# Kernel optimization log

Measured on AMD Instinct MI355X. Metric: run time of the kernel, lower is better.

## Reference

```python
import jax, jax.numpy as jnp
import numpy as np

T, B, D, H = 1024, 256, 256, 256


def setup_inputs() -> dict:
    key = jax.random.key(0)
    k1, k2, k3, k4 = jax.random.split(key, 4)
    ins = jax.random.normal(k1, (T, B, D), dtype=jnp.float32)
    resets = jax.random.randint(k2, (T, B), 0, 2).astype(jnp.bool_)
    init_h = jnp.zeros((B, H), dtype=jnp.float32)
    # packed GRU weights in (r, z, n) order; flax GRUCell: input dense has no
    # bias, hidden dense has bias, and r gates (Wh_n @ h + b_n).
    Wi = jax.random.normal(k3, (D, 3 * H), dtype=jnp.float32) / np.sqrt(D)
    Wh = jax.random.normal(k4, (H, 3 * H), dtype=jnp.float32) / np.sqrt(H)
    b = jnp.zeros((3 * H,), dtype=jnp.float32)
    return {"ins": ins, "resets": resets, "init_h": init_h,
            "Wi": Wi, "Wh": Wh, "b": b}


def reference(ins, resets, init_h, Wi, Wh, b):
    def step(h, xt):
        x, reset = xt                                  # x: [B,D], reset: [B]
        h = jnp.where(reset[:, None], jnp.zeros_like(h), h)
        gi = x @ Wi                                    # [B,3H] (no input bias)
        gh = h @ Wh + b                                # [B,3H] (hidden bias)
        ir, iz, i_n = jnp.split(gi, 3, axis=-1)
        hr, hz, h_n = jnp.split(gh, 3, axis=-1)
        r = jax.nn.sigmoid(ir + hr)
        z = jax.nn.sigmoid(iz + hz)
        n = jnp.tanh(i_n + r * h_n)                    # r gates (Wh_n h + b_n)
        new_h = (1.0 - z) * n + z * h
        return new_h, new_h                            # GRU: y == new hidden

    h_final, ys = jax.lax.scan(step, init_h, (ins, resets))
    return ys                                          # [T,B,H]
```

## Files before the change

kernel.cpp:

```cpp
#include <hip/hip_runtime.h>


typedef __attribute__((ext_vector_type(8))) short sv8;
typedef __attribute__((ext_vector_type(4))) short sv4;
typedef __attribute__((ext_vector_type(4))) float fv4;

#define HPAD 264
#define GAP 40

static __device__ __forceinline__ unsigned short f2bf(float f) {
  unsigned int u = __float_as_uint(f);
  u += 0x7fffu + ((u >> 16) & 1u);
  return (unsigned short)(u >> 16);
}
static __device__ __forceinline__ float bf2f(unsigned short s) {
  return __uint_as_float(((unsigned int)s) << 16);
}

__global__ __launch_bounds__(256) void transpose_w(
    const float* __restrict__ Wi, const float* __restrict__ Wh,
    unsigned short* __restrict__ Wt, unsigned short* __restrict__ Wht) {
  __shared__ float tile[32][33];
  const int bid = blockIdx.x;
  const float* src = (bid < 192) ? Wi : Wh;
  unsigned short* dst = (bid < 192) ? Wt : Wht;
  const int local = bid % 192;
  const int c0 = (local % 24) * 32;
  const int k0 = (local / 24) * 32;
  const int t = threadIdx.x, tr = t >> 5, tc = t & 31;
#pragma unroll
  for (int p = 0; p < 4; ++p) {
    int k = tr + p * 8;
    tile[k][tc] = src[(size_t)(k0 + k) * 768 + c0 + tc];
  }
  __syncthreads();
#pragma unroll
  for (int p = 0; p < 4; ++p) {
    int c = tr + p * 8;
    dst[(size_t)(c0 + c) * 256 + k0 + tc] = f2bf(tile[tc][c]);
  }
}

__global__ __launch_bounds__(256) void gi_gemm(
    const float* __restrict__ ins, const unsigned short* __restrict__ Wt,
    unsigned short* __restrict__ gi, int w0) {
  __shared__ __align__(16) unsigned short As[128][GAP];
  __shared__ __align__(16) unsigned short Bs[128][GAP];
  const int t = threadIdx.x;
  const int m0 = blockIdx.x * 128;
  const int n0 = blockIdx.y * 128;
  const int wave = t >> 6, lane = t & 63;
  const int n16 = lane & 15, quad = lane >> 4;
  const int m0w = (wave & 1) * 64, n0w = (wave >> 1) * 64;

  fv4 acc[4][4] = {};
  for (int kb = 0; kb < 8; ++kb) {
#pragma unroll
    for (int r = 0; r < 4; ++r) {
      const int m = (t >> 3) + r * 32;
      const int kk = (t & 7) * 4;
      const int grow = m0 + m;
      const float* xp = ins + ((size_t)(w0 + (grow >> 8)) * 256 + (grow & 255)) * 256 + kb * 32 + kk;
      fv4 v = *(const fv4*)xp;
      sv4 pk = {(short)f2bf(v[0]), (short)f2bf(v[1]), (short)f2bf(v[2]), (short)f2bf(v[3])};
      *(sv4*)&As[m][kk] = pk;
    }
    {
      const int n = t >> 1, kh = (t & 1) * 16;
      const sv8* wp = (const sv8*)(Wt + (size_t)(n0 + n) * 256 + kb * 32 + kh);
      *(sv8*)&Bs[n][kh] = wp[0];
      *(sv8*)&Bs[n][kh + 8] = wp[1];
    }
    __syncthreads();
    sv8 af[4], bfr[4];
#pragma unroll
    for (int mt = 0; mt < 4; ++mt) af[mt] = *(const sv8*)&As[m0w + mt * 16 + n16][quad * 8];
#pragma unroll
    for (int nt = 0; nt < 4; ++nt) bfr[nt] = *(const sv8*)&Bs[n0w + nt * 16 + n16][quad * 8];
#pragma unroll
    for (int mt = 0; mt < 4; ++mt)
#pragma unroll
      for (int nt = 0; nt < 4; ++nt)
        acc[mt][nt] = __builtin_amdgcn_mfma_f32_16x16x32_bf16(af[mt], bfr[nt], acc[mt][nt], 0, 0, 0);
    __syncthreads();
  }
#pragma unroll
  for (int mt = 0; mt < 4; ++mt)
#pragma unroll
    for (int i = 0; i < 4; ++i) {
      const int row = m0 + m0w + mt * 16 + quad * 4 + i;
      unsigned short* gp = gi + (size_t)row * 768 + n0 + n0w + n16;
#pragma unroll
      for (int nt = 0; nt < 4; ++nt) gp[nt * 16] = f2bf(acc[mt][nt][i]);
    }
}

__global__ __launch_bounds__(512, 2) void rec_kernel(
    const unsigned short* __restrict__ gi,
    const int* __restrict__ resets,
    const float* __restrict__ h_in,
    float* __restrict__ h_carry,
    const unsigned short* __restrict__ Wht,
    const float* __restrict__ bias,
    float* __restrict__ out,
    int t0, int wsteps) {
  __shared__ __align__(16) unsigned short whn[256][HPAD];
  __shared__ __align__(16) unsigned short hbuf[2][16][HPAD];
  __shared__ int rstl[1024];
  __shared__ int cand[16];
  __shared__ int cstart[17];
  __shared__ int s_smax;

  const int tid = threadIdx.x;
  const int wave = tid >> 6, lane = tid & 63;
  const int n16 = lane & 15, quad = lane >> 4;
  const int b = blockIdx.x;
  const int wcb = wave * 16;

  for (int e = tid; e < 8192; e += 512) {
    const int col = e >> 5, kc = (e & 31) * 8;
    *(sv8*)&whn[col][kc] = *(const sv8*)(Wht + (size_t)(512 + col) * 256 + kc);
  }
  for (int e = tid; e < wsteps; e += 512)
    rstl[e] = resets[(size_t)(t0 + e) * 256 + b];
  if (tid < 16) cand[tid] = wsteps;
  __syncthreads();

  {
    int span = wsteps >> 4;
    if (span < 1) span = 1;
    for (int e = tid; e < wsteps; e += 512)
      if (rstl[e]) {
        const int j = e / span;
        if (j < 16) atomicMin(&cand[j], e);
      }
  }
  {
    const int row = tid >> 5, c8 = (tid & 31) * 8;
    sv8 pk = {0, 0, 0, 0, 0, 0, 0, 0};
    if (row == 0 && !rstl[0]) {
      fv4 v0 = *(const fv4*)(h_in + (size_t)b * 256 + c8);
      fv4 v1 = *(const fv4*)(h_in + (size_t)b * 256 + c8 + 4);
#pragma unroll
      for (int j = 0; j < 4; ++j) pk[j] = (short)f2bf(v0[j]);
#pragma unroll
      for (int j = 0; j < 4; ++j) pk[4 + j] = (short)f2bf(v1[j]);
    }
    *(sv8*)&hbuf[0][row][c8] = pk;
  }
  __syncthreads();
  if (tid == 0) {
    int span = wsteps >> 4;
    if (span < 1) span = 1;
    int S[17];
    S[16] = wsteps;
    for (int j = 15; j >= 0; --j) S[j] = (cand[j] < wsteps) ? cand[j] : S[j + 1];
    int cnt = 1;
    cstart[0] = 0;
    for (int r = 1; r < 16; ++r) {
      const int v = S[r];
      if (v < wsteps && v > cstart[cnt - 1]) cstart[cnt++] = v;
    }
    for (int r = cnt; r <= 16; ++r) cstart[r] = wsteps;
    int mx = 0;
    for (int r = 0; r < 16; ++r) {
      const int L = cstart[r + 1] - cstart[r];
      if (L > mx) mx = L;
    }
    s_smax = mx;
  }
  __syncthreads();

  int rs_[4], rl_[4];
#pragma unroll
  for (int i = 0; i < 4; ++i) {
    const int ri = quad * 4 + i;
    rs_[i] = cstart[ri];
    rl_[i] = cstart[ri + 1] - rs_[i];
  }
  float hprev[4][2];
#pragma unroll
  for (int i = 0; i < 4; ++i)
#pragma unroll
    for (int c = 0; c < 2; ++c)
      hprev[i][c] = (rs_[i] == 0) ? h_in[(size_t)b * 256 + c * 128 + wcb + n16] : 0.f;

  sv8 whf[2][2][8];
#pragma unroll
  for (int g = 0; g < 2; ++g)
#pragma unroll
    for (int c = 0; c < 2; ++c)
#pragma unroll
      for (int kt = 0; kt < 8; ++kt)
        whf[g][c][kt] = *(const sv8*)(Wht + (size_t)(g * 256 + c * 128 + wcb + n16) * 256 + kt * 32 + quad * 8);

  float b_r[2], b_z[2], b_n[2];
#pragma unroll
  for (int c = 0; c < 2; ++c) {
    const int col = c * 128 + wcb + n16;
    b_r[c] = bias[col];
    b_z[c] = bias[256 + col];
    b_n[c] = bias[512 + col];
  }

  const unsigned short* gbase = gi + (size_t)b * 768 + wcb + n16;
  float* ob0 = out + (size_t)t0 * 65536 + (size_t)b * 256 + wcb + n16;
  const int smax = s_smax;

  auto prefetch = [&](int s, unsigned short (&dst)[2][3][4]) {
#pragma unroll
    for (int i = 0; i < 4; ++i) {
      int lt = rs_[i] + s;
      if (lt > wsteps - 1) lt = wsteps - 1;
      const unsigned short* g0 = gbase + (size_t)lt * 196608;
#pragma unroll
      for (int c = 0; c < 2; ++c) {
        dst[c][0][i] = g0[c * 128];
        dst[c][1][i] = g0[c * 128 + 256];
        dst[c][2][i] = g0[c * 128 + 512];
      }
    }
  };

  auto step = [&](int s, unsigned short (&cur)[2][3][4], unsigned short (&nxt)[2][3][4]) {
    const int rb = s & 1, wb = rb ^ 1;
    fv4 acc[3][2] = {};
#pragma unroll
    for (int kt = 0; kt < 8; ++kt) {
      sv8 hf = *(const sv8*)&hbuf[rb][n16][kt * 32 + quad * 8];
#pragma unroll
      for (int c = 0; c < 2; ++c) {
        sv8 wnf = *(const sv8*)&whn[c * 128 + wcb + n16][kt * 32 + quad * 8];
        acc[0][c] = __builtin_amdgcn_mfma_f32_16x16x32_bf16(hf, whf[0][c][kt], acc[0][c], 0, 0, 0);
        acc[1][c] = __builtin_amdgcn_mfma_f32_16x16x32_bf16(hf, whf[1][c][kt], acc[1][c], 0, 0, 0);
        acc[2][c] = __builtin_amdgcn_mfma_f32_16x16x32_bf16(hf, wnf, acc[2][c], 0, 0, 0);
      }
    }
    prefetch(s + 1, nxt);
#pragma unroll
    for (int i = 0; i < 4; ++i) {
      const int lt = rs_[i] + s;
      const bool act = (s < rl_[i]);
      const int rcur = act ? rstl[lt] : 1;
      const int nf = (s + 1 < rl_[i]) ? rstl[lt + 1] : 1;
#pragma unroll
      for (int c = 0; c < 2; ++c) {
        const float pre_r = bf2f(cur[c][0][i]) + acc[0][c][i] + b_r[c];
        const float pre_z = bf2f(cur[c][1][i]) + acc[1][c][i] + b_z[c];
        const float r = __builtin_amdgcn_rcpf(1.f + __expf(-pre_r));
        const float z = __builtin_amdgcn_rcpf(1.f + __expf(-pre_z));
        const float npre = bf2f(cur[c][2][i]) + r * (acc[2][c][i] + b_n[c]);
        const float n = 1.f - 2.f * __builtin_amdgcn_rcpf(1.f + __expf(2.f * npre));
        const float hp = rcur ? 0.f : hprev[i][c];
        const float hnew = (1.f - z) * n + z * hp;
        hprev[i][c] = hnew;
        if (act) {
          ob0[(size_t)lt * 65536 + c * 128] = hnew;
          if (lt == wsteps - 1) h_carry[(size_t)b * 256 + c * 128 + wcb + n16] = hnew;
        }
        hbuf[wb][quad * 4 + i][c * 128 + wcb + n16] = nf ? (unsigned short)0 : f2bf(hnew);
      }
    }
    __builtin_amdgcn_sched_barrier(0);
    asm volatile("s_waitcnt lgkmcnt(0)" ::: "memory");
    __builtin_amdgcn_s_barrier();
    __builtin_amdgcn_sched_barrier(0);
  };

  unsigned short A_[2][3][4], B_[2][3][4];
  prefetch(0, A_);
  for (int s = 0; s < smax; s += 2) {
    step(s, A_, B_);
    if (s + 1 < smax) step(s + 1, B_, A_);
  }
}

extern "C" void kernel_launch(void* const* d_in, const int* in_sizes, int n_in,
                              void* d_out, int out_size, void* d_ws, size_t ws_size,
                              hipStream_t stream) {
  const float* ins    = (const float*)d_in[0];
  const int* resets   = (const int*)d_in[1];
  const float* init_h = (const float*)d_in[2];
  const float* Wi     = (const float*)d_in[3];
  const float* Wh     = (const float*)d_in[4];
  const float* bias   = (const float*)d_in[5];
  float* out          = (float*)d_out;

  char* ws = (char*)d_ws;
  unsigned short* Wt  = (unsigned short*)ws;
  unsigned short* Wht = (unsigned short*)(ws + 393216);
  float* h_carry      = (float*)(ws + 786432);
  unsigned short* gi  = (unsigned short*)(ws + 1048576);

  int wsteps = 1024;
  while (wsteps > 2 && (size_t)1048576 + (size_t)wsteps * 256 * 768 * 2 > ws_size) wsteps >>= 1;
  const int nwin = 1024 / wsteps;

  hipLaunchKernelGGL(transpose_w, dim3(384), dim3(256), 0, stream, Wi, Wh, Wt, Wht);
  for (int w = 0; w < nwin; ++w) {
    const int t0 = w * wsteps;
    hipLaunchKernelGGL(gi_gemm, dim3(wsteps * 2, 6), dim3(256), 0, stream, ins, Wt, gi, t0);
    hipLaunchKernelGGL(rec_kernel, dim3(256), dim3(512), 0, stream,
                       gi, resets, (w == 0 ? init_h : h_carry), h_carry, Wht, bias, out, t0, wsteps);
  }
}
```

Baseline: 1.062 ms.

## Pre-convert inputs to bf16, use direct global-to-LDS loads, defer recurrence stores

Adds a separate pass that converts the fp32 inputs to bf16 once. The input-projection GEMM now stages tiles with global_load_lds directly into a blocked LDS layout and swaps the grid axes so neighbouring blocks share A rows. In the recurrent kernel, gate prefetch uses incrementing pointers, the reset flag is carried between steps, and output and h_carry stores are moved after the barrier so they stay off the critical path. The trade is an extra 128MB of workspace and a full read/write pass over the inputs, and the workspace check may shrink the window size.

```diff
diff --git a/kernel.cpp b/kernel.cpp
--- a/kernel.cpp
+++ b/kernel.cpp
@@ -6,7 +6,6 @@
 typedef __attribute__((ext_vector_type(4))) float fv4;
 
 #define HPAD 264
-#define GAP 40
 
 static __device__ __forceinline__ unsigned short f2bf(float f) {
   unsigned int u = __float_as_uint(f);
@@ -15,6 +14,12 @@
 }
 static __device__ __forceinline__ float bf2f(unsigned short s) {
   return __uint_as_float(((unsigned int)s) << 16);
+}
+
+static __device__ __forceinline__ void gload16(const void* g, void* l) {
+  __builtin_amdgcn_global_load_lds((__attribute__((address_space(1))) void*)g,
+                                   (__attribute__((address_space(3))) void*)l,
+                                   16, 0, 0);
 }
 
 __global__ __launch_bounds__(256) void transpose_w(
@@ -41,42 +46,61 @@
   }
 }
 
-__global__ __launch_bounds__(256) void gi_gemm(
-    const float* __restrict__ ins, const unsigned short* __restrict__ Wt,
+__global__ __launch_bounds__(256) void conv_bf16(
+    const float* __restrict__ src, unsigned short* __restrict__ dst, int n8) {
+  int i = blockIdx.x * 256 + threadIdx.x;
+  const int stride = gridDim.x * 256;
+  for (; i < n8; i += stride) {
+    fv4 a = *(const fv4*)(src + (size_t)i * 8);
+    fv4 b = *(const fv4*)(src + (size_t)i * 8 + 4);
+    sv8 o = {(short)f2bf(a[0]), (short)f2bf(a[1]), (short)f2bf(a[2]), (short)f2bf(a[3]),
+             (short)f2bf(b[0]), (short)f2bf(b[1]), (short)f2bf(b[2]), (short)f2bf(b[3])};
+    *(sv8*)(dst + (size_t)i * 8) = o;
+  }
+}
+
+__global__ __launch_bounds__(256) void gi_gemm2(
+    const unsigned short* __restrict__ insb,
+    const unsigned short* __restrict__ Wt,
     unsigned short* __restrict__ gi, int w0) {
-  __shared__ __align__(16) unsigned short As[128][GAP];
-  __shared__ __align__(16) unsigned short Bs[128][GAP];
+  __shared__ __align__(16) unsigned short As[4096];
+  __shared__ __align__(16) unsigned short Bs[4096];
   const int t = threadIdx.x;
-  const int m0 = blockIdx.x * 128;
-  const int n0 = blockIdx.y * 128;
   const int wave = t >> 6, lane = t & 63;
   const int n16 = lane & 15, quad = lane >> 4;
+  const int n0 = blockIdx.x * 128;
+  const int m0 = blockIdx.y * 128;
   const int m0w = (wave & 1) * 64, n0w = (wave >> 1) * 64;
+
+  const int c0i = wave * 128 + lane;
+  const int c1i = c0i + 64;
+  const int r0 = ((c0i >> 5) << 3) | (c0i & 7), k0c = ((c0i >> 3) & 3) * 8;
+  const int r1 = ((c1i >> 5) << 3) | (c1i & 7), k1c = ((c1i >> 3) & 3) * 8;
+  unsigned short* ldA0 = As + (size_t)(wave * 2) * 512;
+  unsigned short* ldA1 = As + (size_t)(wave * 2 + 1) * 512;
+  unsigned short* ldB0 = Bs + (size_t)(wave * 2) * 512;
+  unsigned short* ldB1 = Bs + (size_t)(wave * 2 + 1) * 512;
+  const unsigned short* gA0 = insb + (size_t)(w0 * 256 + m0 + r0) * 256 + k0c;
+  const unsigned short* gA1 = insb + (size_t)(w0 * 256 + m0 + r1) * 256 + k1c;
+  const unsigned short* gB0 = Wt + (size_t)(n0 + r0) * 256 + k0c;
+  const unsigned short* gB1 = Wt + (size_t)(n0 + r1) * 256 + k1c;
+
+  const int arow = m0w + n16, brow = n0w + n16;
+  const char* apb = (const char*)As + ((arow >> 3) << 9) + (quad << 7) + ((arow & 7) << 4);
+  const char* bpb = (const char*)Bs + ((brow >> 3) << 9) + (quad << 7) + ((brow & 7) << 4);
 
   fv4 acc[4][4] = {};
   for (int kb = 0; kb < 8; ++kb) {
-#pragma unroll
-    for (int r = 0; r < 4; ++r) {
-      const int m = (t >> 3) + r * 32;
-      const int kk = (t & 7) * 4;
-      const int grow = m0 + m;
-      const float* xp = ins + ((size_t)(w0 + (grow >> 8)) * 256 + (grow & 255)) * 256 + kb * 32 + kk;
-      fv4 v = *(const fv4*)xp;
-      sv4 pk = {(short)f2bf(v[0]), (short)f2bf(v[1]), (short)f2bf(v[2]), (short)f2bf(v[3])};
-      *(sv4*)&As[m][kk] = pk;
-    }
-    {
-      const int n = t >> 1, kh = (t & 1) * 16;
-      const sv8* wp = (const sv8*)(Wt + (size_t)(n0 + n) * 256 + kb * 32 + kh);
-      *(sv8*)&Bs[n][kh] = wp[0];
-      *(sv8*)&Bs[n][kh + 8] = wp[1];
-    }
+    gload16(gA0 + kb * 32, ldA0);
+    gload16(gA1 + kb * 32, ldA1);
+    gload16(gB0 + kb * 32, ldB0);
+    gload16(gB1 + kb * 32, ldB1);
     __syncthreads();
     sv8 af[4], bfr[4];
 #pragma unroll
-    for (int mt = 0; mt < 4; ++mt) af[mt] = *(const sv8*)&As[m0w + mt * 16 + n16][quad * 8];
-#pragma unroll
-    for (int nt = 0; nt < 4; ++nt) bfr[nt] = *(const sv8*)&Bs[n0w + nt * 16 + n16][quad * 8];
+    for (int mt = 0; mt < 4; ++mt) af[mt] = *(const sv8*)(apb + mt * 1024);
+#pragma unroll
+    for (int nt = 0; nt < 4; ++nt) bfr[nt] = *(const sv8*)(bpb + nt * 1024);
 #pragma unroll
     for (int mt = 0; mt < 4; ++mt)
 #pragma unroll
@@ -150,8 +174,6 @@
   }
   __syncthreads();
   if (tid == 0) {
-    int span = wsteps >> 4;
-    if (span < 1) span = 1;
     int S[17];
     S[16] = wsteps;
     for (int j = 15; j >= 0; --j) S[j] = (cand[j] < wsteps) ? cand[j] : S[j + 1];
@@ -203,24 +225,29 @@
     b_n[c] = bias[512 + col];
   }
 
-  const unsigned short* gbase = gi + (size_t)b * 768 + wcb + n16;
+  const size_t boff = (size_t)b * 768 + wcb + n16;
+  const unsigned short* pmax = gi + (size_t)(wsteps - 1) * 196608 + boff;
+  const unsigned short* gp[4];
+#pragma unroll
+  for (int i = 0; i < 4; ++i) {
+    const int r0 = (rs_[i] < wsteps) ? rs_[i] : (wsteps - 1);
+    gp[i] = gi + (size_t)r0 * 196608 + boff;
+  }
   float* ob0 = out + (size_t)t0 * 65536 + (size_t)b * 256 + wcb + n16;
   const int smax = s_smax;
 
-  auto prefetch = [&](int s, unsigned short (&dst)[2][3][4]) {
-#pragma unroll
-    for (int i = 0; i < 4; ++i) {
-      int lt = rs_[i] + s;
-      if (lt > wsteps - 1) lt = wsteps - 1;
-      const unsigned short* g0 = gbase + (size_t)lt * 196608;
-#pragma unroll
-      for (int c = 0; c < 2; ++c) {
-        dst[c][0][i] = g0[c * 128];
-        dst[c][1][i] = g0[c * 128 + 256];
-        dst[c][2][i] = g0[c * 128 + 512];
-      }
-    }
-  };
+  unsigned short A_[2][3][4], B_[2][3][4];
+#pragma unroll
+  for (int i = 0; i < 4; ++i)
+#pragma unroll
+    for (int c = 0; c < 2; ++c) {
+      A_[c][0][i] = gp[i][c * 128];
+      A_[c][1][i] = gp[i][c * 128 + 256];
+      A_[c][2][i] = gp[i][c * 128 + 512];
+    }
+  int rc[4];
+#pragma unroll
+  for (int i = 0; i < 4; ++i) rc[i] = (rl_[i] > 0) ? rstl[rs_[i]] : 1;
 
   auto step = [&](int s, unsigned short (&cur)[2][3][4], unsigned short (&nxt)[2][3][4]) {
     const int rb = s & 1, wb = rb ^ 1;
@@ -236,13 +263,25 @@
         acc[2][c] = __builtin_amdgcn_mfma_f32_16x16x32_bf16(hf, wnf, acc[2][c], 0, 0, 0);
       }
     }
-    prefetch(s + 1, nxt);
 #pragma unroll
     for (int i = 0; i < 4; ++i) {
-      const int lt = rs_[i] + s;
-      const bool act = (s < rl_[i]);
-      const int rcur = act ? rstl[lt] : 1;
-      const int nf = (s + 1 < rl_[i]) ? rstl[lt + 1] : 1;
+      gp[i] += 196608;
+      if (gp[i] > pmax) gp[i] = pmax;
+#pragma unroll
+      for (int c = 0; c < 2; ++c) {
+        nxt[c][0][i] = gp[i][c * 128];
+        nxt[c][1][i] = gp[i][c * 128 + 256];
+        nxt[c][2][i] = gp[i][c * 128 + 512];
+      }
+    }
+    int nf[4], lt[4];
+    bool act[4];
+    float hnew[4][2];
+#pragma unroll
+    for (int i = 0; i < 4; ++i) {
+      lt[i] = rs_[i] + s;
+      act[i] = (s < rl_[i]);
+      nf[i] = (s + 1 < rl_[i]) ? rstl[lt[i] + 1] : 1;
 #pragma unroll
       for (int c = 0; c < 2; ++c) {
         const float pre_r = bf2f(cur[c][0][i]) + acc[0][c][i] + b_r[c];
@@ -251,24 +290,31 @@
         const float z = __builtin_amdgcn_rcpf(1.f + __expf(-pre_z));
         const float npre = bf2f(cur[c][2][i]) + r * (acc[2][c][i] + b_n[c]);
         const float n = 1.f - 2.f * __builtin_amdgcn_rcpf(1.f + __expf(2.f * npre));
-        const float hp = rcur ? 0.f : hprev[i][c];
-        const float hnew = (1.f - z) * n + z * hp;
-        hprev[i][c] = hnew;
-        if (act) {
-          ob0[(size_t)lt * 65536 + c * 128] = hnew;
-          if (lt == wsteps - 1) h_carry[(size_t)b * 256 + c * 128 + wcb + n16] = hnew;
-        }
-        hbuf[wb][quad * 4 + i][c * 128 + wcb + n16] = nf ? (unsigned short)0 : f2bf(hnew);
+        const float hp = rc[i] ? 0.f : hprev[i][c];
+        const float h = (1.f - z) * n + z * hp;
+        hnew[i][c] = h;
+        hprev[i][c] = h;
+        hbuf[wb][quad * 4 + i][c * 128 + wcb + n16] = nf[i] ? (unsigned short)0 : f2bf(h);
       }
     }
     __builtin_amdgcn_sched_barrier(0);
     asm volatile("s_waitcnt lgkmcnt(0)" ::: "memory");
     __builtin_amdgcn_s_barrier();
     __builtin_amdgcn_sched_barrier(0);
+#pragma unroll
+    for (int i = 0; i < 4; ++i) {
+      if (act[i]) {
+#pragma unroll
+        for (int c = 0; c < 2; ++c) {
+          ob0[(size_t)lt[i] * 65536 + c * 128] = hnew[i][c];
+          if (lt[i] == wsteps - 1)
+            h_carry[(size_t)b * 256 + c * 128 + wcb + n16] = hnew[i][c];
+        }
+      }
+      rc[i] = nf[i];
+    }
   };
 
-  unsigned short A_[2][3][4], B_[2][3][4];
-  prefetch(0, A_);
   for (int s = 0; s < smax; s += 2) {
     step(s, A_, B_);
     if (s + 1 < smax) step(s + 1, B_, A_);
@@ -287,19 +333,22 @@
   float* out          = (float*)d_out;
 
   char* ws = (char*)d_ws;
-  unsigned short* Wt  = (unsigned short*)ws;
-  unsigned short* Wht = (unsigned short*)(ws + 393216);
-  float* h_carry      = (float*)(ws + 786432);
-  unsigned short* gi  = (unsigned short*)(ws + 1048576);
+  unsigned short* Wt   = (unsigned short*)ws;
+  unsigned short* Wht  = (unsigned short*)(ws + 393216);
+  float* h_carry       = (float*)(ws + 786432);
+  unsigned short* insb = (unsigned short*)(ws + 1048576);
+  const size_t gi_off  = 1048576 + 134217728;
+  unsigned short* gi   = (unsigned short*)(ws + gi_off);
 
   int wsteps = 1024;
-  while (wsteps > 2 && (size_t)1048576 + (size_t)wsteps * 256 * 768 * 2 > ws_size) wsteps >>= 1;
+  while (wsteps > 2 && gi_off + (size_t)wsteps * 256 * 768 * 2 > ws_size) wsteps >>= 1;
   const int nwin = 1024 / wsteps;
 
   hipLaunchKernelGGL(transpose_w, dim3(384), dim3(256), 0, stream, Wi, Wh, Wt, Wht);
+  hipLaunchKernelGGL(conv_bf16, dim3(2048), dim3(256), 0, stream, ins, insb, 8388608);
   for (int w = 0; w < nwin; ++w) {
     const int t0 = w * wsteps;
-    hipLaunchKernelGGL(gi_gemm, dim3(wsteps * 2, 6), dim3(256), 0, stream, ins, Wt, gi, t0);
+    hipLaunchKernelGGL(gi_gemm2, dim3(6, wsteps * 2), dim3(256), 0, stream, insb, Wt, gi, t0);
     hipLaunchKernelGGL(rec_kernel, dim3(256), dim3(512), 0, stream,
                        gi, resets, (w == 0 ? init_h : h_carry), h_carry, Wht, bias, out, t0, wsteps);
   }
```

Measured after the change: 931.7 us. 1.14x faster.
